# Performance work log

Hardware: AMD Instinct MI355X
Metric: run time of the kernel (lower is better)

The kernel has to match this reference:

```python
import jax, jax.numpy as jnp
import numpy as np

B, T, C, H = 2, 2048, 1024, 16
D = C // H  # head dim, even
NEG = -1e10  # masked_fill value used by the torch module (not -inf)


def _rope_cache(dim, max_positions):
    # Faithful to source: theta_i = 1/10000**(-2*(i-1)/dim), i = arange(dim//2)
    i = jnp.arange(dim // 2, dtype=jnp.float32)
    theta = 1.0 / (10000.0 ** (-2.0 * (i - 1.0) / dim))
    ang = jnp.arange(max_positions, dtype=jnp.float32)[:, None] * theta[None, :]  # [T, D/2]
    return jnp.cos(ang), jnp.sin(ang)


def _apply_rope(x, cos, sin):
    # x: [B,H,T,D]; consecutive pairs form complex numbers (x[...,2j], x[...,2j+1])
    xp = x.reshape(*x.shape[:-1], D // 2, 2)
    xr, xi = xp[..., 0], xp[..., 1]
    rr = xr * cos - xi * sin
    ri = xr * sin + xi * cos
    return jnp.stack([rr, ri], axis=-1).reshape(x.shape)


def setup_inputs() -> dict:
    key = jax.random.key(0)
    ks = jax.random.split(key, 5)
    s = 1.0 / np.sqrt(C)
    return {
        'x': jax.random.normal(ks[0], (B, T, C), jnp.float32),
        'Wq': jax.random.normal(ks[1], (C, C), jnp.float32) * s,
        'bq': jnp.zeros((C,), jnp.float32),
        'Wk': jax.random.normal(ks[2], (C, C), jnp.float32) * s,
        'bk': jnp.zeros((C,), jnp.float32),
        'Wv': jax.random.normal(ks[3], (C, C), jnp.float32) * s,
        'bv': jnp.zeros((C,), jnp.float32),
        'Wp': jax.random.normal(ks[4], (C, C), jnp.float32) * s,
        'bp': jnp.zeros((C,), jnp.float32),
    }


def reference(x, Wq, bq, Wk, bk, Wv, bv, Wp, bp):
    cos, sin = _rope_cache(D, T)  # [T, D/2]
    def split_heads(h):
        return h.reshape(B, T, H, D).transpose(0, 2, 1, 3)  # [B,H,T,D]
    q = split_heads(x @ Wq.T + bq)
    k = split_heads(x @ Wk.T + bk)
    v = split_heads(x @ Wv.T + bv)
    q = _apply_rope(q, cos, sin)
    k = _apply_rope(k, cos, sin)
    att = jnp.einsum('bhqd,bhkd->bhqk', q, k) * (1.0 / np.sqrt(D))  # [B,H,T,T]
    causal = jnp.tril(jnp.ones((T, T), bool))
    att = jnp.where(causal, att, NEG)
    att = jax.nn.softmax(att, axis=-1)
    y = jnp.einsum('bhqk,bhkd->bhqd', att, v)
    y = y.transpose(0, 2, 1, 3).reshape(B, T, C)
    return y @ Wp.T + bp
```

## Files before the change

### kernel.cpp

```cpp
#include <hip/hip_runtime.h>

#define SEQ 2048
#define CDIM 1024
#define NHEAD 16
#define HDIM 64

typedef __bf16 bf16x8 __attribute__((ext_vector_type(8)));
typedef __bf16 bf16x4v __attribute__((ext_vector_type(4)));
typedef float f32x4 __attribute__((ext_vector_type(4)));

typedef const __attribute__((address_space(1))) char* gcp_t;
typedef __attribute__((address_space(3))) char* lcp_t;

__device__ __forceinline__ void gload16(const void* g, void* l) {
    __builtin_amdgcn_global_load_lds((gcp_t)g, (lcp_t)l, 16, 0, 0);
}

__device__ __forceinline__ unsigned short f2bf(float f) {
    unsigned int u = __float_as_uint(f);
    u += 0x7fffu + ((u >> 16) & 1u);
    return (unsigned short)(u >> 16);
}

__device__ __forceinline__ int swz16(int r) { return ((r >> 1) & 3) << 4; }


__global__ void cvt_kernel(const float* __restrict__ src, unsigned short* __restrict__ dst, int n4) {
    int i = blockIdx.x * blockDim.x + threadIdx.x;
    if (i < n4) {
        float4 v = ((const float4*)src)[i];
        ushort4 o;
        o.x = f2bf(v.x); o.y = f2bf(v.y); o.z = f2bf(v.z); o.w = f2bf(v.w);
        ((ushort4*)dst)[i] = o;
    }
}

__global__ void cvtw_kernel(const float* __restrict__ Wq, const float* __restrict__ Wk,
                            const float* __restrict__ Wv, const float* __restrict__ Wp,
                            unsigned short* __restrict__ wqkv, unsigned short* __restrict__ wpb) {
    int i = blockIdx.x * blockDim.x + threadIdx.x;
    int which = i >> 18, r = i & 262143;
    const float* s = (which == 0) ? Wq : (which == 1) ? Wk : (which == 2) ? Wv : Wp;
    unsigned short* d = (which < 3) ? (wqkv + (size_t)which * 1048576) : wpb;
    float4 v = ((const float4*)s)[r];
    ushort4 o;
    o.x = f2bf(v.x); o.y = f2bf(v.y); o.z = f2bf(v.z); o.w = f2bf(v.w);
    ((ushort4*)d)[r] = o;
}

__global__ void rope_kernel(float2* __restrict__ cstab) {
    int idx = blockIdx.x * blockDim.x + threadIdx.x;
    int j = idx & 31, t = idx >> 5;
    float e = -2.0f * ((float)j - 1.0f) / 64.0f;
    float denom = (float)pow(10000.0, (double)e);
    float theta = 1.0f / denom;
    float ang = (float)t * theta;
    cstab[idx] = make_float2(cosf(ang), sinf(ang));
}

__global__ __launch_bounds__(512, 1) void gemm_qkv256(
    const unsigned short* __restrict__ A, const unsigned short* __restrict__ Bm,
    const float* __restrict__ b0, const float* __restrict__ b1, const float* __restrict__ b2,
    unsigned short* __restrict__ qb, unsigned short* __restrict__ kb,
    unsigned short* __restrict__ vtb, const float2* __restrict__ cstab)
{
    constexpr int NT = 16;
    constexpr int NXT = 12, CPX = 24;
    __shared__ __align__(16) char As[2][256 * 128];
    __shared__ __align__(16) char Bs[2][256 * 128];
    const int tid = threadIdx.x, lane = tid & 63, wid = tid >> 6;
    const int wr = wid >> 2, wc = wid & 3;
    const int bid = blockIdx.x;
    const int swz = (bid & 7) * CPX + (bid >> 3);
    const int mt = swz / NXT;
    const int m0 = mt * 256, n0 = (swz - mt * NXT) * 256;

    f32x4 acc[8][4] = {};

    const char* Ag = (const char*)A + (size_t)m0 * 2048;
    const char* Bg = (const char*)Bm + (size_t)n0 * 2048;
    const int r0 = tid >> 3, cb = (tid & 7) * 16;

    auto stageA = [&](int k0, int bufi, int s) {
        const int r = r0 + 64 * s;
        gload16(Ag + (size_t)r * 2048 + k0 * 2 + (cb ^ ((r & 7) << 4)),
                As[bufi] + s * 8192 + wid * 1024);
    };
    auto stageB = [&](int k0, int bufi, int s) {
        const int r = r0 + 64 * s;
        gload16(Bg + (size_t)r * 2048 + k0 * 2 + (cb ^ ((r & 7) << 4)),
                Bs[bufi] + s * 8192 + wid * 1024);
    };

#pragma unroll
    for (int s = 0; s < 4; ++s) { stageA(0, 0, s); stageB(0, 0, s); }
    asm volatile("s_waitcnt vmcnt(0)" ::: "memory");
    __builtin_amdgcn_s_barrier();

    for (int t = 0; t < NT; ++t) {
        const int cur = t & 1;
        const char* Ac = As[cur];
        const char* Bc = Bs[cur];
        const int k1 = (t + 1) * 64;
        bf16x8 bfr[4][2];
#pragma unroll
        for (int p = 0; p < 4; ++p) {
            if (p == 0) {
#pragma unroll
                for (int fc = 0; fc < 4; ++fc)
#pragma unroll
                    for (int kf = 0; kf < 2; ++kf) {
                        const int r = wc * 64 + fc * 16 + (lane & 15);
                        bfr[fc][kf] = *(const bf16x8*)(Bc + r * 128 + ((kf * 64 + (lane >> 4) * 16) ^ ((r & 7) << 4)));
                    }
            }
            bf16x8 af[2][2];
#pragma unroll
            for (int fa = 0; fa < 2; ++fa)
#pragma unroll
                for (int kf = 0; kf < 2; ++kf) {
                    const int r = wr * 128 + (p * 2 + fa) * 16 + (lane & 15);
                    af[fa][kf] = *(const bf16x8*)(Ac + r * 128 + ((kf * 64 + (lane >> 4) * 16) ^ ((r & 7) << 4)));
                }
            if (t + 1 < NT) { stageA(k1, cur ^ 1, p); stageB(k1, cur ^ 1, p); }
            __builtin_amdgcn_s_barrier();
            __builtin_amdgcn_s_setprio(1);
#pragma unroll
            for (int kf = 0; kf < 2; ++kf)
#pragma unroll
                for (int fa = 0; fa < 2; ++fa)
#pragma unroll
                    for (int fc = 0; fc < 4; ++fc)
                        acc[p * 2 + fa][fc] = __builtin_amdgcn_mfma_f32_16x16x32_bf16(
                            af[fa][kf], bfr[fc][kf], acc[p * 2 + fa][fc], 0, 0, 0);
            __builtin_amdgcn_s_setprio(0);
        }
        asm volatile("s_waitcnt vmcnt(0)" ::: "memory");
        __builtin_amdgcn_s_barrier();
    }

    const float QSCL = 0.18033688011112042f;
#pragma unroll
    for (int fc = 0; fc < 4; ++fc) {
        const int ng = n0 + wc * 64 + fc * 16 + (lane & 15);
        const int which = ng >> 10, nl = ng & 1023;
        const int h = nl >> 6, d = nl & 63;
        const float* bptr = (which == 0) ? b0 : (which == 1) ? b1 : b2;
        const float bias = bptr[nl];
        if (which < 2) {
            unsigned short* dst = (which == 0) ? qb : kb;
            const float qs = (which == 0) ? QSCL : 1.0f;
            const int j = d >> 1;
#pragma unroll
            for (int fr = 0; fr < 8; ++fr) {
#pragma unroll
                for (int i = 0; i < 4; ++i) {
                    const int row = m0 + wr * 128 + fr * 16 + (lane >> 4) * 4 + i;
                    const int bb = row >> 11, tt = row & 2047;
                    float v = acc[fr][fc][i] + bias;
                    float pp = __shfl_xor(v, 1);
                    const float2 cs = cstab[tt * 32 + j];
                    v = (d & 1) ? fmaf(v, cs.x, pp * cs.y) : fmaf(v, cs.x, -pp * cs.y);
                    dst[((size_t)((bb * 16 + h) * 2048 + tt)) * 64 + d] = f2bf(v * qs);
                }
            }
        } else {
#pragma unroll
            for (int fr = 0; fr < 8; ++fr) {
                const int rowb = m0 + wr * 128 + fr * 16 + (lane >> 4) * 4;
                const int bb = rowb >> 11, tt = rowb & 2047;
                ushort4 pk;
                pk.x = f2bf(acc[fr][fc][0] + bias);
                pk.y = f2bf(acc[fr][fc][1] + bias);
                pk.z = f2bf(acc[fr][fc][2] + bias);
                pk.w = f2bf(acc[fr][fc][3] + bias);
                *(ushort4*)(vtb + ((size_t)((bb * 16 + h) * 64 + d)) * 2048 + tt) = pk;
            }
        }
    }
}

template <int MODE, int BM>
__global__ __launch_bounds__(256) void gemm_bt(
    const unsigned short* __restrict__ A, const unsigned short* __restrict__ Bm,
    const float* __restrict__ b0,
    float* __restrict__ outf)
{
    constexpr int K = 1024;
    constexpr int NIT = K / 32;
    constexpr int NR = (BM == 128) ? 4 : 2;
    __shared__ __align__(16) char As[2][BM * 64];
    __shared__ __align__(16) char Bs[2][128 * 64];
    const int tid = threadIdx.x, lane = tid & 63, wid = tid >> 6;
    const int m0 = blockIdx.y * BM, n0 = blockIdx.x * 128;
    const int wr = (BM == 128) ? ((wid >> 1) * 64) : 0;
    const int wc = (BM == 128) ? ((wid & 1) * 64) : (wid * 32);

    f32x4 acc[4][NR] = {};

    const char* Ag = (const char*)(A + (size_t)m0 * K);
    const char* Bg = (const char*)(Bm + (size_t)n0 * K);
    const int r0 = tid >> 2, cb = (tid & 3) * 16;
    const int ldsw = wid << 10;

    auto stage = [&](int k0, int bufi) {
        char* Ad = As[bufi];
        char* Bd = Bs[bufi];
        gload16(Ag + (size_t)r0 * 2048 + k0 * 2 + (cb ^ swz16(r0)), Ad + ldsw);
        if constexpr (BM == 128)
            gload16(Ag + (size_t)(r0 + 64) * 2048 + k0 * 2 + (cb ^ swz16(r0 + 64)), Ad + 4096 + ldsw);
        gload16(Bg + (size_t)r0 * 2048 + k0 * 2 + (cb ^ swz16(r0)), Bd + ldsw);
        gload16(Bg + (size_t)(r0 + 64) * 2048 + k0 * 2 + (cb ^ swz16(r0 + 64)), Bd + 4096 + ldsw);
    };

    stage(0, 0);
    __syncthreads();

    for (int it = 0; it < NIT; ++it) {
        const int cur = it & 1;
        if (it + 1 < NIT) stage((it + 1) * 32, cur ^ 1);
        const char* Ac = As[cur];
        const char* Bc = Bs[cur];
        const int fs = (lane >> 4) * 16;
        bf16x8 af[4], bfr[NR];
#pragma unroll
        for (int am = 0; am < 4; ++am) {
            const int r = wr + am * 16 + (lane & 15);
            af[am] = *(const bf16x8*)(Ac + r * 64 + (fs ^ swz16(r)));
        }
#pragma unroll
        for (int an = 0; an < NR; ++an) {
            const int r = wc + an * 16 + (lane & 15);
            bfr[an] = *(const bf16x8*)(Bc + r * 64 + (fs ^ swz16(r)));
        }
#pragma unroll
        for (int am = 0; am < 4; ++am)
#pragma unroll
            for (int an = 0; an < NR; ++an)
                acc[am][an] = __builtin_amdgcn_mfma_f32_16x16x32_bf16(af[am], bfr[an], acc[am][an], 0, 0, 0);
        __syncthreads();
    }

#pragma unroll
    for (int an = 0; an < NR; ++an) {
        const int col = n0 + wc + an * 16 + (lane & 15);
        const float bias = b0[col];
#pragma unroll
        for (int am = 0; am < 4; ++am)
#pragma unroll
            for (int i = 0; i < 4; ++i) {
                const int row = m0 + wr + am * 16 + (lane >> 4) * 4 + i;
                outf[(size_t)row * 1024 + col] = acc[am][an][i] + bias;
            }
    }
}

__global__ __launch_bounds__(256) void attn_kernel(
    const unsigned short* __restrict__ qb, const unsigned short* __restrict__ kb,
    const unsigned short* __restrict__ vtb, unsigned short* __restrict__ yb)
{
    __shared__ __align__(16) unsigned short Ks[2][64 * 64];
    __shared__ __align__(16) unsigned short Vs[2][64 * 64];
    __shared__ __align__(16) unsigned short Ps[4][16 * 64];
    const int tid = threadIdx.x, lane = tid & 63, wid = tid >> 6;
    const int bh = blockIdx.y;
    const int b = bh >> 4, h = bh & 15;
    const int qt = (bh & 16) ? (31 - blockIdx.x) : blockIdx.x;
    const int q0 = qt * 64;
    const int qw = q0 + wid * 16;
    const unsigned short* Qg = qb + (size_t)bh * SEQ * HDIM;
    const char* Kg = (const char*)(kb + (size_t)bh * SEQ * HDIM);
    const char* Vg = (const char*)(vtb + (size_t)bh * HDIM * SEQ);

    bf16x8 qf[2];
#pragma unroll
    for (int kf = 0; kf < 2; ++kf)
        qf[kf] = *(const bf16x8*)(Qg + (size_t)(qw + (lane & 15)) * 64 + kf * 32 + (lane >> 4) * 8);

    f32x4 o[4] = {};
    float mrun = -3e38f;
    float lrun = 0.0f;

    const int nt = qt + 1;
    const int cr0 = tid >> 3, cc0 = ((tid & 7) * 16) ^ ((cr0 & 7) << 4);
    const int cr1 = cr0 + 32, cc1 = ((tid & 7) * 16) ^ ((cr1 & 7) << 4);
    const int ldsw = wid << 10;

    auto stage = [&](int kt, int bufi) {
        const size_t kv0 = (size_t)kt * 64;
        gload16(Kg + (kv0 + cr0) * 128 + cc0, (char*)Ks[bufi] + ldsw);
        gload16(Kg + (kv0 + cr1) * 128 + cc1, (char*)Ks[bufi] + 4096 + ldsw);
        gload16(Vg + (size_t)cr0 * 4096 + kv0 * 2 + cc0, (char*)Vs[bufi] + ldsw);
        gload16(Vg + (size_t)cr1 * 4096 + kv0 * 2 + cc1, (char*)Vs[bufi] + 4096 + ldsw);
    };

    stage(0, 0);
    __syncthreads();

    for (int kt = 0; kt < nt; ++kt) {
        const int cur = kt & 1;
        if (kt + 1 < nt) stage(kt + 1, cur ^ 1);
        const int kv0 = kt * 64;
        {
            f32x4 s[4] = {};
            __builtin_amdgcn_s_setprio(1);
#pragma unroll
            for (int kf = 0; kf < 2; ++kf) {
                bf16x8 kfr[4];
#pragma unroll
                for (int an = 0; an < 4; ++an) {
                    const int r = an * 16 + (lane & 15);
                    kfr[an] = *(const bf16x8*)((const char*)Ks[cur] + r * 128 + ((kf * 64 + (lane >> 4) * 16) ^ ((r & 7) << 4)));
                }
#pragma unroll
                for (int an = 0; an < 4; ++an)
                    s[an] = __builtin_amdgcn_mfma_f32_16x16x32_bf16(kfr[an], qf[kf], s[an], 0, 0, 0);
            }
            __builtin_amdgcn_s_setprio(0);
            const bool need_mask = (kv0 + 63 > qw);
            const int qg = qw + (lane & 15);
            const int kbase = kv0 + ((lane >> 4) << 2);
            float p[4][4];
            float mx = -3e38f;
#pragma unroll
            for (int an = 0; an < 4; ++an)
#pragma unroll
                for (int i = 0; i < 4; ++i) {
                    float v = s[an][i];
                    if (need_mask && (kbase + an * 16 + i > qg)) v = -3e38f;
                    p[an][i] = v;
                    mx = fmaxf(mx, v);
                }
            mx = fmaxf(mx, __shfl_xor(mx, 16));
            mx = fmaxf(mx, __shfl_xor(mx, 32));
            if (!__all(mx <= mrun + 8.0f)) {
                const float mnew = fmaxf(mrun, mx);
                const float fsc = __builtin_amdgcn_exp2f(mrun - mnew);
                lrun *= fsc;
#pragma unroll
                for (int dn = 0; dn < 4; ++dn) o[dn] *= fsc;
                mrun = mnew;
            }
            float rs = 0.0f;
#pragma unroll
            for (int an = 0; an < 4; ++an)
#pragma unroll
                for (int i = 0; i < 4; ++i) {
                    p[an][i] = __builtin_amdgcn_exp2f(p[an][i] - mrun);
                    rs += p[an][i];
                }
            rs += __shfl_xor(rs, 16);
            rs += __shfl_xor(rs, 32);
            lrun += rs;
            const int ql = lane & 15;
            char* pbs = (char*)Ps[wid] + ql * 128;
            const int xr = (ql & 7) << 4;
            const int gb = (lane >> 4) << 3;
#pragma unroll
            for (int an = 0; an < 4; ++an) {
                bf16x4v pk;
                pk[0] = (__bf16)p[an][0]; pk[1] = (__bf16)p[an][1];
                pk[2] = (__bf16)p[an][2]; pk[3] = (__bf16)p[an][3];
                *(bf16x4v*)(pbs + ((an * 32 + gb) ^ xr)) = pk;
            }
            __builtin_amdgcn_s_setprio(1);
#pragma unroll
            for (int kf = 0; kf < 2; ++kf) {
                bf16x8 vf[4], pf;
#pragma unroll
                for (int dn = 0; dn < 4; ++dn) {
                    const int r = dn * 16 + (lane & 15);
                    vf[dn] = *(const bf16x8*)((const char*)Vs[cur] + r * 128 + ((kf * 64 + (lane >> 4) * 16) ^ ((r & 7) << 4)));
                }
                {
                    const int qlr = lane & 15;
                    pf = *(const bf16x8*)((const char*)Ps[wid] + qlr * 128 + ((kf * 64 + (lane >> 4) * 16) ^ ((qlr & 7) << 4)));
                }
#pragma unroll
                for (int dn = 0; dn < 4; ++dn)
                    o[dn] = __builtin_amdgcn_mfma_f32_16x16x32_bf16(vf[dn], pf, o[dn], 0, 0, 0);
            }
            __builtin_amdgcn_s_setprio(0);
        }
        __syncthreads();
    }

    {
        const float inv = 1.0f / lrun;
        const int qg = qw + (lane & 15);
        unsigned short* yrow = yb + (size_t)(b * SEQ + qg) * CDIM + h * 64;
#pragma unroll
        for (int dn = 0; dn < 4; ++dn) {
            const int d = dn * 16 + ((lane >> 4) << 2);
            bf16x4v pk;
            pk[0] = (__bf16)(o[dn][0] * inv);
            pk[1] = (__bf16)(o[dn][1] * inv);
            pk[2] = (__bf16)(o[dn][2] * inv);
            pk[3] = (__bf16)(o[dn][3] * inv);
            *(bf16x4v*)(yrow + d) = pk;
        }
    }
}


extern "C" void kernel_launch(void* const* d_in, const int* in_sizes, int n_in,
                              void* d_out, int out_size, void* d_ws, size_t ws_size,
                              hipStream_t stream) {
    (void)in_sizes; (void)n_in; (void)out_size; (void)ws_size;
    const float* x  = (const float*)d_in[0];
    const float* Wq = (const float*)d_in[1];
    const float* bq = (const float*)d_in[2];
    const float* Wk = (const float*)d_in[3];
    const float* bk = (const float*)d_in[4];
    const float* Wv = (const float*)d_in[5];
    const float* bv = (const float*)d_in[6];
    const float* Wp = (const float*)d_in[7];
    const float* bp = (const float*)d_in[8];
    float* out = (float*)d_out;

    char* ws = (char*)d_ws;
    size_t off = 0;
    auto take = [&](size_t bytes) -> char* {
        char* p = ws + off;
        off = (off + bytes + 255) & ~(size_t)255;
        return p;
    };
    float2* cstab = (float2*)take((size_t)SEQ * 32 * 8);
    unsigned short* xb   = (unsigned short*)take((size_t)4096 * 1024 * 2);
    unsigned short* wqkv = (unsigned short*)take((size_t)3 * 1024 * 1024 * 2);
    unsigned short* wpb  = (unsigned short*)take((size_t)1024 * 1024 * 2);
    unsigned short* qbuf = (unsigned short*)take((size_t)32 * SEQ * HDIM * 2);
    unsigned short* kbuf = (unsigned short*)take((size_t)32 * SEQ * HDIM * 2);
    unsigned short* vtb  = (unsigned short*)take((size_t)32 * HDIM * SEQ * 2);
    unsigned short* yb   = (unsigned short*)take((size_t)4096 * 1024 * 2);

    rope_kernel<<<256, 256, 0, stream>>>(cstab);
    cvt_kernel<<<4096, 256, 0, stream>>>(x, xb, 1048576);
    cvtw_kernel<<<4096, 256, 0, stream>>>(Wq, Wk, Wv, Wp, wqkv, wpb);

    gemm_qkv256<<<192, 512, 0, stream>>>(xb, wqkv, bq, bk, bv, qbuf, kbuf, vtb, cstab);
    dim3 g1(32, 32);
    attn_kernel<<<g1, 256, 0, stream>>>(qbuf, kbuf, vtb, yb);
    dim3 g2(8, 64);
    gemm_bt<1, 64><<<g2, 256, 0, stream>>>(yb, wpb, bp, out);
}
```

Baseline: 134.2 us.

## Retile QKV GEMM to 256x192 tiles filling 256 CUs, merge convert kernels

The QKV projection GEMM moves from 256x256 tiles on 192 blocks to 256x192 tiles on 256 blocks, so the grid matches the MI355X CU count and no CUs sit idle. Staging now issues all next-tile loads at the top of each k-step instead of interleaving them across sub-phases. The A fragments are re-read per row-fragment inside the kf loop, with fewer intermediate barriers. The x and weight bf16 conversion kernels are merged into one launch. Tradeoffs are a lower MFMA-to-load ratio per tile and the loss of the fine-grained load/compute interleave.

```diff
diff --git a/kernel.cpp b/kernel.cpp
--- a/kernel.cpp
+++ b/kernel.cpp
@@ -25,23 +25,22 @@
 __device__ __forceinline__ int swz16(int r) { return ((r >> 1) & 3) << 4; }
 
 
-__global__ void cvt_kernel(const float* __restrict__ src, unsigned short* __restrict__ dst, int n4) {
+__global__ void cvt_all(const float* __restrict__ x,
+                        const float* __restrict__ Wq, const float* __restrict__ Wk,
+                        const float* __restrict__ Wv, const float* __restrict__ Wp,
+                        unsigned short* __restrict__ xb,
+                        unsigned short* __restrict__ wqkv, unsigned short* __restrict__ wpb) {
     int i = blockIdx.x * blockDim.x + threadIdx.x;
-    if (i < n4) {
-        float4 v = ((const float4*)src)[i];
-        ushort4 o;
-        o.x = f2bf(v.x); o.y = f2bf(v.y); o.z = f2bf(v.z); o.w = f2bf(v.w);
-        ((ushort4*)dst)[i] = o;
-    }
-}
-
-__global__ void cvtw_kernel(const float* __restrict__ Wq, const float* __restrict__ Wk,
-                            const float* __restrict__ Wv, const float* __restrict__ Wp,
-                            unsigned short* __restrict__ wqkv, unsigned short* __restrict__ wpb) {
-    int i = blockIdx.x * blockDim.x + threadIdx.x;
-    int which = i >> 18, r = i & 262143;
-    const float* s = (which == 0) ? Wq : (which == 1) ? Wk : (which == 2) ? Wv : Wp;
-    unsigned short* d = (which < 3) ? (wqkv + (size_t)which * 1048576) : wpb;
+    const float* s;
+    unsigned short* d;
+    int r;
+    if (i < 1048576) { s = x; d = xb; r = i; }
+    else {
+        int j = i - 1048576;
+        int which = j >> 18; r = j & 262143;
+        s = (which == 0) ? Wq : (which == 1) ? Wk : (which == 2) ? Wv : Wp;
+        d = (which < 3) ? (wqkv + (size_t)which * 1048576) : wpb;
+    }
     float4 v = ((const float4*)s)[r];
     ushort4 o;
     o.x = f2bf(v.x); o.y = f2bf(v.y); o.z = f2bf(v.z); o.w = f2bf(v.w);
@@ -58,81 +57,69 @@
     cstab[idx] = make_float2(cosf(ang), sinf(ang));
 }
 
-__global__ __launch_bounds__(512, 1) void gemm_qkv256(
+__global__ __launch_bounds__(512, 1) void gemm_qkv(
     const unsigned short* __restrict__ A, const unsigned short* __restrict__ Bm,
     const float* __restrict__ b0, const float* __restrict__ b1, const float* __restrict__ b2,
     unsigned short* __restrict__ qb, unsigned short* __restrict__ kb,
     unsigned short* __restrict__ vtb, const float2* __restrict__ cstab)
 {
     constexpr int NT = 16;
-    constexpr int NXT = 12, CPX = 24;
     __shared__ __align__(16) char As[2][256 * 128];
-    __shared__ __align__(16) char Bs[2][256 * 128];
+    __shared__ __align__(16) char Bs2[2][192 * 128];
     const int tid = threadIdx.x, lane = tid & 63, wid = tid >> 6;
     const int wr = wid >> 2, wc = wid & 3;
     const int bid = blockIdx.x;
-    const int swz = (bid & 7) * CPX + (bid >> 3);
-    const int mt = swz / NXT;
-    const int m0 = mt * 256, n0 = (swz - mt * NXT) * 256;
-
-    f32x4 acc[8][4] = {};
+    const int swz = (bid & 7) * 32 + (bid >> 3);
+    const int mt = swz >> 4, ntl = swz & 15;
+    const int m0 = mt * 256, n0 = ntl * 192;
+
+    f32x4 acc[8][3] = {};
 
     const char* Ag = (const char*)A + (size_t)m0 * 2048;
     const char* Bg = (const char*)Bm + (size_t)n0 * 2048;
     const int r0 = tid >> 3, cb = (tid & 7) * 16;
 
-    auto stageA = [&](int k0, int bufi, int s) {
-        const int r = r0 + 64 * s;
-        gload16(Ag + (size_t)r * 2048 + k0 * 2 + (cb ^ ((r & 7) << 4)),
-                As[bufi] + s * 8192 + wid * 1024);
+    auto stage = [&](int k0, int bufi) {
+#pragma unroll
+        for (int v = 0; v < 4; ++v) {
+            const int r = r0 + 64 * v;
+            gload16(Ag + (size_t)r * 2048 + k0 * 2 + (cb ^ ((r & 7) << 4)),
+                    As[bufi] + v * 8192 + wid * 1024);
+        }
+#pragma unroll
+        for (int v = 0; v < 3; ++v) {
+            const int r = r0 + 64 * v;
+            gload16(Bg + (size_t)r * 2048 + k0 * 2 + (cb ^ ((r & 7) << 4)),
+                    Bs2[bufi] + v * 8192 + wid * 1024);
+        }
     };
-    auto stageB = [&](int k0, int bufi, int s) {
-        const int r = r0 + 64 * s;
-        gload16(Bg + (size_t)r * 2048 + k0 * 2 + (cb ^ ((r & 7) << 4)),
-                Bs[bufi] + s * 8192 + wid * 1024);
-    };
-
-#pragma unroll
-    for (int s = 0; s < 4; ++s) { stageA(0, 0, s); stageB(0, 0, s); }
+
+    stage(0, 0);
     asm volatile("s_waitcnt vmcnt(0)" ::: "memory");
     __builtin_amdgcn_s_barrier();
 
     for (int t = 0; t < NT; ++t) {
         const int cur = t & 1;
+        if (t + 1 < NT) stage((t + 1) * 64, cur ^ 1);
         const char* Ac = As[cur];
-        const char* Bc = Bs[cur];
-        const int k1 = (t + 1) * 64;
-        bf16x8 bfr[4][2];
-#pragma unroll
-        for (int p = 0; p < 4; ++p) {
-            if (p == 0) {
-#pragma unroll
-                for (int fc = 0; fc < 4; ++fc)
-#pragma unroll
-                    for (int kf = 0; kf < 2; ++kf) {
-                        const int r = wc * 64 + fc * 16 + (lane & 15);
-                        bfr[fc][kf] = *(const bf16x8*)(Bc + r * 128 + ((kf * 64 + (lane >> 4) * 16) ^ ((r & 7) << 4)));
-                    }
-            }
-            bf16x8 af[2][2];
-#pragma unroll
-            for (int fa = 0; fa < 2; ++fa)
-#pragma unroll
-                for (int kf = 0; kf < 2; ++kf) {
-                    const int r = wr * 128 + (p * 2 + fa) * 16 + (lane & 15);
-                    af[fa][kf] = *(const bf16x8*)(Ac + r * 128 + ((kf * 64 + (lane >> 4) * 16) ^ ((r & 7) << 4)));
-                }
-            if (t + 1 < NT) { stageA(k1, cur ^ 1, p); stageB(k1, cur ^ 1, p); }
-            __builtin_amdgcn_s_barrier();
+        const char* Bc = Bs2[cur];
+#pragma unroll
+        for (int kf = 0; kf < 2; ++kf) {
+            bf16x8 bfr[3];
+#pragma unroll
+            for (int fc = 0; fc < 3; ++fc) {
+                const int r = wc * 48 + fc * 16 + (lane & 15);
+                bfr[fc] = *(const bf16x8*)(Bc + r * 128 + ((kf * 64 + (lane >> 4) * 16) ^ ((r & 7) << 4)));
+            }
             __builtin_amdgcn_s_setprio(1);
 #pragma unroll
-            for (int kf = 0; kf < 2; ++kf)
-#pragma unroll
-                for (int fa = 0; fa < 2; ++fa)
-#pragma unroll
-                    for (int fc = 0; fc < 4; ++fc)
-                        acc[p * 2 + fa][fc] = __builtin_amdgcn_mfma_f32_16x16x32_bf16(
-                            af[fa][kf], bfr[fc][kf], acc[p * 2 + fa][fc], 0, 0, 0);
+            for (int fr = 0; fr < 8; ++fr) {
+                const int r = wr * 128 + fr * 16 + (lane & 15);
+                bf16x8 af = *(const bf16x8*)(Ac + r * 128 + ((kf * 64 + (lane >> 4) * 16) ^ ((r & 7) << 4)));
+#pragma unroll
+                for (int fc = 0; fc < 3; ++fc)
+                    acc[fr][fc] = __builtin_amdgcn_mfma_f32_16x16x32_bf16(af, bfr[fc], acc[fr][fc], 0, 0, 0);
+            }
             __builtin_amdgcn_s_setprio(0);
         }
         asm volatile("s_waitcnt vmcnt(0)" ::: "memory");
@@ -141,8 +128,8 @@
 
     const float QSCL = 0.18033688011112042f;
 #pragma unroll
-    for (int fc = 0; fc < 4; ++fc) {
-        const int ng = n0 + wc * 64 + fc * 16 + (lane & 15);
+    for (int fc = 0; fc < 3; ++fc) {
+        const int ng = n0 + wc * 48 + fc * 16 + (lane & 15);
         const int which = ng >> 10, nl = ng & 1023;
         const int h = nl >> 6, d = nl & 63;
         const float* bptr = (which == 0) ? b0 : (which == 1) ? b1 : b2;
@@ -435,10 +422,9 @@
     unsigned short* yb   = (unsigned short*)take((size_t)4096 * 1024 * 2);
 
     rope_kernel<<<256, 256, 0, stream>>>(cstab);
-    cvt_kernel<<<4096, 256, 0, stream>>>(x, xb, 1048576);
-    cvtw_kernel<<<4096, 256, 0, stream>>>(Wq, Wk, Wv, Wp, wqkv, wpb);
-
-    gemm_qkv256<<<192, 512, 0, stream>>>(xb, wqkv, bq, bk, bv, qbuf, kbuf, vtb, cstab);
+    cvt_all<<<8192, 256, 0, stream>>>(x, Wq, Wk, Wv, Wp, xb, wqkv, wpb);
+
+    gemm_qkv<<<256, 512, 0, stream>>>(xb, wqkv, bq, bk, bv, qbuf, kbuf, vtb, cstab);
     dim3 g1(32, 32);
     attn_kernel<<<g1, 256, 0, stream>>>(qbuf, kbuf, vtb, yb);
     dim3 g2(8, 64);
```

Measured after the change: 130.8 us. 1.03x faster.
